# Optimization experiments

Hardware: AMD Instinct MI355X
Metric: run time of the kernel (lower is better)

## Reference

```python
import jax, jax.numpy as jnp
import numpy as np
from jax import lax
from jax.scipy.special import logsumexp

N = 1024   # keypoints image 0
M = 1024   # keypoints image 1
D = 256    # descriptor dim
H = 4      # attention heads
L = 18     # GNN layers ('self','cross')*9
ITERS = 100
KENC = [4, 32, 64, 128, 256]


def conv1(x, w, b):
    # 1x1 Conv1d == channel matmul: x [b,c,n], w [o,c], b [o]
    return jnp.einsum('oc,bcn->bon', w, x) + b[None, :, None]


def inorm(x, eps=1e-5):
    # InstanceNorm1d (affine=False): normalize over length per (b, c)
    m = jnp.mean(x, axis=-1, keepdims=True)
    v = jnp.var(x, axis=-1, keepdims=True)
    return (x - m) * lax.rsqrt(v + eps)


def attention_block(x, src, pw, pb, mw, mb):
    b, d, _ = x.shape
    dh = d // H
    q = conv1(x, pw[0], pb[0]).reshape(b, dh, H, -1)
    k = conv1(src, pw[1], pb[1]).reshape(b, dh, H, -1)
    v = conv1(src, pw[2], pb[2]).reshape(b, dh, H, -1)
    s = jnp.einsum('bdhn,bdhm->bhnm', q, k) / (dh ** 0.5)
    p = jax.nn.softmax(s, axis=-1)
    o = jnp.einsum('bhnm,bdhm->bdhn', p, v).reshape(b, d, -1)
    return conv1(o, mw, mb)


def prop(x, src, i, Pw, Pb, Mw, Mb, W0, B0, W1, B1):
    msg = attention_block(x, src, Pw[i], Pb[i], Mw[i], Mb[i])
    h = jnp.concatenate([x, msg], axis=1)          # [b, 2D, n]
    h = jax.nn.relu(inorm(conv1(h, W0[i], B0[i])))
    return conv1(h, W1[i], B1[i])


def sinkhorn(Z, log_mu, log_nu, iters):
    def step(carry, _):
        u, v = carry
        u = log_mu - logsumexp(Z + v[:, None, :], axis=2)
        v = log_nu - logsumexp(Z + u[:, :, None], axis=1)
        return (u, v), None
    init = (jnp.zeros_like(log_mu), jnp.zeros_like(log_nu))
    (u, v), _ = lax.scan(jax.checkpoint(step), init, None, length=iters)
    return Z + u[:, :, None] + v[:, None, :]


def log_optimal_transport(scores, alpha, iters):
    b, m, n = scores.shape
    bins0 = jnp.broadcast_to(alpha, (b, m, 1))
    bins1 = jnp.broadcast_to(alpha, (b, 1, n))
    binsA = jnp.broadcast_to(alpha, (b, 1, 1))
    couplings = jnp.concatenate([
        jnp.concatenate([scores, bins0], axis=-1),
        jnp.concatenate([bins1, binsA], axis=-1)], axis=1)  # [b, m+1, n+1]
    norm = np.float32(-np.log(m + n))
    log_mu = jnp.concatenate([jnp.full((m,), norm, scores.dtype),
                              jnp.array([np.log(n)], scores.dtype) + norm])
    log_nu = jnp.concatenate([jnp.full((n,), norm, scores.dtype),
                              jnp.array([np.log(m)], scores.dtype) + norm])
    log_mu = jnp.broadcast_to(log_mu[None], (b, m + 1))
    log_nu = jnp.broadcast_to(log_nu[None], (b, n + 1))
    Z = sinkhorn(couplings, log_mu, log_nu, iters)
    return Z - norm


def setup_inputs() -> dict:
    key = jax.random.key(0)
    ks = iter(jax.random.split(key, 64))
    w = lambda shape, s=0.02: jax.random.normal(next(ks), shape, jnp.float32) * s
    inp = {
        'keypoints0': jax.random.normal(next(ks), (1, N, 3), jnp.float32),
        'keypoints1': jax.random.normal(next(ks), (1, M, 3), jnp.float32),
        'descriptors0': jax.random.normal(next(ks), (1, D, N), jnp.float32),
        'descriptors1': jax.random.normal(next(ks), (1, D, M), jnp.float32),
        'scores0': jax.random.uniform(next(ks), (1, N), jnp.float32),
        'scores1': jax.random.uniform(next(ks), (1, M), jnp.float32),
    }
    for i in range(4):
        inp[f'kenc_w{i}'] = w((KENC[i + 1], KENC[i]), 0.1)
        inp[f'kenc_b{i}'] = jnp.zeros((KENC[i + 1],), jnp.float32)
    inp['gnn_proj_w'] = w((L, 3, D, D))
    inp['gnn_proj_b'] = jnp.zeros((L, 3, D), jnp.float32)
    inp['gnn_merge_w'] = w((L, D, D))
    inp['gnn_merge_b'] = jnp.zeros((L, D), jnp.float32)
    inp['gnn_mlp_w0'] = w((L, 2 * D, 2 * D))
    inp['gnn_mlp_b0'] = jnp.zeros((L, 2 * D), jnp.float32)
    inp['gnn_mlp_w1'] = w((L, D, 2 * D))
    inp['gnn_mlp_b1'] = jnp.zeros((L, D), jnp.float32)
    inp['final_w'] = w((D, D))
    inp['final_b'] = jnp.zeros((D,), jnp.float32)
    inp['bin_score'] = jnp.float32(1.0)
    return inp


def reference(keypoints0, keypoints1, descriptors0, descriptors1, scores0, scores1,
              kenc_w0, kenc_b0, kenc_w1, kenc_b1, kenc_w2, kenc_b2, kenc_w3, kenc_b3,
              gnn_proj_w, gnn_proj_b, gnn_merge_w, gnn_merge_b,
              gnn_mlp_w0, gnn_mlp_b0, gnn_mlp_w1, gnn_mlp_b1,
              final_w, final_b, bin_score):
    def kenc(kpts, sc):
        h = jnp.concatenate([jnp.swapaxes(kpts, 1, 2), sc[:, None, :]], axis=1)  # [b,4,n]
        h = jax.nn.relu(inorm(conv1(h, kenc_w0, kenc_b0)))
        h = jax.nn.relu(inorm(conv1(h, kenc_w1, kenc_b1)))
        h = jax.nn.relu(inorm(conv1(h, kenc_w2, kenc_b2)))
        return conv1(h, kenc_w3, kenc_b3)

    d0 = descriptors0 + kenc(keypoints0, scores0)
    d1 = descriptors1 + kenc(keypoints1, scores1)
    for i in range(L):  # even: self, odd: cross
        cross = (i % 2 == 1)
        s0 = d1 if cross else d0
        s1 = d0 if cross else d1
        delta0 = prop(d0, s0, i, gnn_proj_w, gnn_proj_b, gnn_merge_w, gnn_merge_b,
                      gnn_mlp_w0, gnn_mlp_b0, gnn_mlp_w1, gnn_mlp_b1)
        delta1 = prop(d1, s1, i, gnn_proj_w, gnn_proj_b, gnn_merge_w, gnn_merge_b,
                      gnn_mlp_w0, gnn_mlp_b0, gnn_mlp_w1, gnn_mlp_b1)
        d0, d1 = d0 + delta0, d1 + delta1
    md0 = conv1(d0, final_w, final_b)
    md1 = conv1(d1, final_w, final_b)
    scores = jnp.einsum('bdn,bdm->bnm', md0, md1) / (D ** 0.5)
    return log_optimal_transport(scores, bin_score, ITERS)
```

## Files before the change

kernel.cpp:

```cpp
#include <hip/hip_runtime.h>
#include <cstddef>

#define TPB 256

typedef _Float16 f16;
typedef _Float16 f16x4 __attribute__((ext_vector_type(4)));
typedef _Float16 f16x8 __attribute__((ext_vector_type(8)));
typedef float f32x4 __attribute__((ext_vector_type(4)));

__device__ __forceinline__ float block_sum(float v, float* red) {
  int tid = threadIdx.x;
  red[tid] = v; __syncthreads();
#pragma unroll
  for (int off = 128; off > 0; off >>= 1) {
    if (tid < off) red[tid] += red[tid + off];
    __syncthreads();
  }
  float r = red[0];
  __syncthreads();
  return r;
}

__global__ __launch_bounds__(TPB) void build_h0(const float* __restrict__ kp0,
                                                const float* __restrict__ kp1,
                                                const float* __restrict__ sc0,
                                                const float* __restrict__ sc1,
                                                float* __restrict__ h0) {
  int n = blockIdx.x * TPB + threadIdx.x;
  int im = blockIdx.y;
  const float* kp = im ? kp1 : kp0;
  const float* sc = im ? sc1 : sc0;
  float* h = h0 + (size_t)im * 4096;
  h[n]        = kp[n * 3 + 0];
  h[1024 + n] = kp[n * 3 + 1];
  h[2048 + n] = kp[n * 3 + 2];
  h[3072 + n] = sc[n];
}

template<bool NORMRELU, bool RESID>
__global__ __launch_bounds__(TPB) void chanconv(const float* __restrict__ W,
                                                const float* __restrict__ bias,
                                                const float* __restrict__ in, long instride,
                                                const float* res0, const float* res1,
                                                float* __restrict__ out, long outstride, int C) {
  int o = blockIdx.x, im = blockIdx.y, tid = threadIdx.x;
  const float* inp = in + (long)im * instride;
  __shared__ float Ws[128];
  __shared__ float red[TPB];
  for (int c = tid; c < C; c += TPB) Ws[c] = W[(long)o * C + c];
  __syncthreads();
  float b = bias[o];
  float4 acc = {b, b, b, b};
  for (int c = 0; c < C; ++c) {
    float w = Ws[c];
    float4 v = *(const float4*)(inp + (long)c * 1024 + tid * 4);
    acc.x += w * v.x; acc.y += w * v.y; acc.z += w * v.z; acc.w += w * v.w;
  }
  float* orow = out + (long)im * outstride + (long)o * 1024;
  if (NORMRELU) {
    float s = acc.x + acc.y + acc.z + acc.w;
    float mean = block_sum(s, red) * (1.f / 1024.f);
    float dx = acc.x - mean, dy = acc.y - mean, dz = acc.z - mean, dw = acc.w - mean;
    float var = block_sum(dx * dx + dy * dy + dz * dz + dw * dw, red) * (1.f / 1024.f);
    float rstd = rsqrtf(var + 1e-5f);
    float4 o4 = {fmaxf(dx * rstd, 0.f), fmaxf(dy * rstd, 0.f),
                 fmaxf(dz * rstd, 0.f), fmaxf(dw * rstd, 0.f)};
    *(float4*)(orow + tid * 4) = o4;
  } else {
    if (RESID) {
      const float* res = im ? res1 : res0;
      float4 r = *(const float4*)(res + (long)o * 1024 + tid * 4);
      acc.x += r.x; acc.y += r.y; acc.z += r.z; acc.w += r.w;
    }
    *(float4*)(orow + tid * 4) = acc;
  }
}

struct GBH {
  const void* A; const void* B; const void* B2; void* C;
  const float* bias; const float* res; const float* mu; const float* rs;
  void* o2a; void* o2b; int coff; int pad;
};
struct GB16 { GBH g[16]; };

#define F_BNORM   1
#define F_BCONCAT 2
#define F_BADD    4
#define F_CD16    8
#define F_RES     16
#define F_OUT2    32
#define F_CSCAT   64

template<int BN, int ASRC, int BSRC, int FLAGS>
__global__ __launch_bounds__(TPB) void gemmh(GB16 gbs, int K, int lda, int ldb,
                                             int ldc, float alpha, int ksplit) {
  constexpr int WN = BN / 2;
  constexpr int NFR = WN / 16;
  GBH g = gbs.g[blockIdx.z];
  const int tid = threadIdx.x;
  const int lane = tid & 63, wid = tid >> 6;
  const int wm = wid >> 1, wn = wid & 1;
  const int m0 = blockIdx.y * 64, n0 = blockIdx.x * BN;
  __shared__ f16 As[64][36];
  __shared__ f16 Bs[BN][36];
  f32x4 acc[2][NFR];
#pragma unroll
  for (int i = 0; i < 2; ++i)
#pragma unroll
    for (int j = 0; j < NFR; ++j) acc[i][j] = (f32x4){0.f, 0.f, 0.f, 0.f};

  for (int k0 = 0; k0 < K; k0 += 32) {
    if constexpr (ASRC == 0) {
      const int m = tid >> 2, k4 = (tid & 3) * 8;
      const float* ap = (const float*)g.A + (long)(m0 + m) * lda + k0 + k4;
      float4 u0 = *(const float4*)ap, u1 = *(const float4*)(ap + 4);
      f16x4 h0 = {(f16)u0.x, (f16)u0.y, (f16)u0.z, (f16)u0.w};
      f16x4 h1 = {(f16)u1.x, (f16)u1.y, (f16)u1.z, (f16)u1.w};
      *(f16x4*)&As[m][k4] = h0;
      *(f16x4*)&As[m][k4 + 4] = h1;
    } else if constexpr (ASRC == 1) {
      const int k = tid >> 3, mg = (tid & 7) * 8;
      const f16* ap = (const f16*)g.A + (long)(k0 + k) * lda + m0 + mg;
      f16x8 h = *(const f16x8*)ap;
#pragma unroll
      for (int j = 0; j < 8; ++j) As[mg + j][k] = h[j];
    } else {
      const int m = tid >> 2, k4 = (tid & 3) * 8;
      const f16* ap = (const f16*)g.A + (long)(m0 + m) * lda + k0 + k4;
      f16x8 h = *(const f16x8*)ap;
      const float M = g.mu[m0 + m], Iv = g.rs[m0 + m];
      f16x4 h0, h1;
#pragma unroll
      for (int j = 0; j < 4; ++j) h0[j] = (f16)(__expf((float)h[j] - M) * Iv);
#pragma unroll
      for (int j = 0; j < 4; ++j) h1[j] = (f16)(__expf((float)h[j + 4] - M) * Iv);
      *(f16x4*)&As[m][k4] = h0;
      *(f16x4*)&As[m][k4 + 4] = h1;
    }
#pragma unroll
    for (int r = 0; r < BN / 64; ++r) {
      if constexpr (BSRC == 0) {
        const int k = tid >> 3, ng = (tid & 7) * 8 + r * 64;
        const int kg = k0 + k;
        const float* bp;
        if constexpr ((FLAGS & F_BCONCAT) != 0)
          bp = (kg < ksplit) ? ((const float*)g.B + (long)kg * ldb)
                             : ((const float*)g.B2 + (long)(kg - ksplit) * ldb);
        else
          bp = (const float*)g.B + (long)kg * ldb;
        float4 u0 = *(const float4*)(bp + n0 + ng);
        float4 u1 = *(const float4*)(bp + n0 + ng + 4);
        Bs[ng + 0][k] = (f16)u0.x; Bs[ng + 1][k] = (f16)u0.y;
        Bs[ng + 2][k] = (f16)u0.z; Bs[ng + 3][k] = (f16)u0.w;
        Bs[ng + 4][k] = (f16)u1.x; Bs[ng + 5][k] = (f16)u1.y;
        Bs[ng + 6][k] = (f16)u1.z; Bs[ng + 7][k] = (f16)u1.w;
      } else if constexpr (BSRC == 1) {
        const int k = tid >> 3, ng = (tid & 7) * 8 + r * 64;
        const int kg = k0 + k;
        f16x8 h = *(const f16x8*)((const f16*)g.B + (long)kg * ldb + n0 + ng);
        if constexpr ((FLAGS & F_BNORM) != 0) {
          const float mu = g.mu[kg], rs = g.rs[kg];
#pragma unroll
          for (int j = 0; j < 8; ++j)
            h[j] = (f16)fmaxf(((float)h[j] - mu) * rs, 0.f);
        }
#pragma unroll
        for (int j = 0; j < 8; ++j) Bs[ng + j][k] = h[j];
      } else {
        const int n = (tid >> 2) + r * 64, k4 = (tid & 3) * 8;
        const f16* bp = (const f16*)g.B + (long)(n0 + n) * ldb + k0 + k4;
        f16x8 h = *(const f16x8*)bp;
        if constexpr ((FLAGS & F_BADD) != 0) {
          f16x8 h2 = *(const f16x8*)((const f16*)g.B2 + (long)(n0 + n) * ldb + k0 + k4);
          h = h + h2;
        }
        f16x4 h0 = {h[0], h[1], h[2], h[3]};
        f16x4 h1 = {h[4], h[5], h[6], h[7]};
        *(f16x4*)&Bs[n][k4] = h0;
        *(f16x4*)&Bs[n][k4 + 4] = h1;
      }
    }
    __syncthreads();
#pragma unroll
    for (int ks = 0; ks < 2; ++ks) {
      const int kof = ks * 16 + ((lane >> 4) << 2);
      f16x4 a[2], b[NFR];
      a[0] = *(const f16x4*)&As[wm * 32 + (lane & 15)][kof];
      a[1] = *(const f16x4*)&As[wm * 32 + 16 + (lane & 15)][kof];
#pragma unroll
      for (int fn = 0; fn < NFR; ++fn)
        b[fn] = *(const f16x4*)&Bs[wn * WN + fn * 16 + (lane & 15)][kof];
#pragma unroll
      for (int fm = 0; fm < 2; ++fm)
#pragma unroll
        for (int fn = 0; fn < NFR; ++fn)
          acc[fm][fn] = __builtin_amdgcn_mfma_f32_16x16x16f16(a[fm], b[fn], acc[fm][fn], 0, 0, 0);
    }
    __syncthreads();
  }

  const int r0 = (lane >> 4) << 2, cn = lane & 15;
#pragma unroll
  for (int fm = 0; fm < 2; ++fm) {
#pragma unroll
    for (int r = 0; r < 4; ++r) {
      const int m = m0 + wm * 32 + fm * 16 + r0 + r;
      const float bi = g.bias ? g.bias[m] : 0.f;
#pragma unroll
      for (int fn = 0; fn < NFR; ++fn) {
        const int n = n0 + wn * WN + fn * 16 + cn;
        float v = acc[fm][fn][r] * alpha + bi;
        if constexpr ((FLAGS & F_RES) != 0) v += g.res[(long)m * ldc + n];
        if constexpr ((FLAGS & F_OUT2) != 0) {
          ((float*)g.C)[(long)m * 1028 + n] = v;
          ((f16*)g.o2a)[(long)m * 1028 + n] = (f16)v;
          ((f16*)g.o2b)[(long)n * 1028 + m] = (f16)v;
        } else if constexpr ((FLAGS & F_CSCAT) != 0) {
          ((f16*)g.C)[(long)m * ldc + g.coff + 4 * n] = (f16)v;
        } else if constexpr ((FLAGS & F_CD16) != 0) {
          ((f16*)g.C)[(long)m * ldc + n] = (f16)v;
        } else {
          ((float*)g.C)[(long)m * ldc + n] = v;
        }
      }
    }
  }
}

__global__ __launch_bounds__(TPB) void rowlse_h(const f16* __restrict__ S,
                                                float* __restrict__ Mrow,
                                                float* __restrict__ Inv) {
  int row = blockIdx.x * 4 + (threadIdx.x >> 6);
  int lane = threadIdx.x & 63;
  const f16x8* p = (const f16x8*)(S + (long)row * 1024);
  f16x8 v0 = p[lane], v1 = p[lane + 64];
  float m = -1e30f;
#pragma unroll
  for (int j = 0; j < 8; ++j)
    m = fmaxf(m, fmaxf((float)v0[j], (float)v1[j]));
#pragma unroll
  for (int off = 32; off > 0; off >>= 1) m = fmaxf(m, __shfl_xor(m, off));
  float s = 0.f;
#pragma unroll
  for (int j = 0; j < 8; ++j)
    s += __expf((float)v0[j] - m) + __expf((float)v1[j] - m);
#pragma unroll
  for (int off = 32; off > 0; off >>= 1) s += __shfl_xor(s, off);
  if (lane == 0) { Mrow[row] = m; Inv[row] = 1.f / s; }
}

__global__ __launch_bounds__(TPB) void rowstats2_h(const f16* __restrict__ t,
                                                   float* __restrict__ mu,
                                                   float* __restrict__ rs) {
  int row = blockIdx.x * 4 + (threadIdx.x >> 6);
  int lane = threadIdx.x & 63;
  const f16x8* p = (const f16x8*)(t + (long)row * 1024);
  f16x8 v0 = p[lane], v1 = p[lane + 64];
  float s = 0.f, s2 = 0.f;
#pragma unroll
  for (int j = 0; j < 8; ++j) {
    float a = (float)v0[j], b = (float)v1[j];
    s += a + b; s2 += a * a + b * b;
  }
#pragma unroll
  for (int off = 32; off > 0; off >>= 1) { s += __shfl_xor(s, off); s2 += __shfl_xor(s2, off); }
  if (lane == 0) {
    float mean = s * (1.f / 1024.f);
    mu[row] = mean;
    rs[row] = rsqrtf(fmaxf(s2 * (1.f / 1024.f) - mean * mean, 0.f) + 1e-5f);
  }
}

#define NORMC  (-7.62461899f)
#define LOGN   (6.93147181f)
#define LOG_MN (7.62461899f)
#define ZLD    1028
#define SINKB  64

__global__ __launch_bounds__(TPB) void fill_bins(float* __restrict__ Z,
                                                 const float* __restrict__ alpha_p,
                                                 float* __restrict__ vb,
                                                 unsigned* __restrict__ bar) {
  float a = *alpha_p;
  int t = blockIdx.x * TPB + threadIdx.x;
  if (t < ZLD) vb[t] = 0.f;
  if (t == 0) *bar = 0u;
  if (t <= 1024) {
    Z[(long)t * ZLD + 1024] = a;
    Z[(long)1024 * ZLD + t] = a;
  }
}

__device__ __forceinline__ float llc_load(const float* p) {
  return __hip_atomic_load(p, __ATOMIC_RELAXED, __HIP_MEMORY_SCOPE_AGENT);
}
__device__ __forceinline__ void llc_store(float* p, float v) {
  __hip_atomic_store(p, v, __ATOMIC_RELAXED, __HIP_MEMORY_SCOPE_AGENT);
}

__device__ __forceinline__ void gridbar(unsigned* __restrict__ bar, unsigned gen) {
  __syncthreads();
  if (threadIdx.x == 0) {
    __hip_atomic_fetch_add(bar, 1u, __ATOMIC_RELAXED, __HIP_MEMORY_SCOPE_AGENT);
    const unsigned target = gen * SINKB;
    while (__hip_atomic_load(bar, __ATOMIC_RELAXED, __HIP_MEMORY_SCOPE_AGENT) < target) {}
  }
  asm volatile("" ::: "memory");
  __syncthreads();
}

__device__ __forceinline__ void sink_half(const f16x8 zreg[4][2],
                                          const float* __restrict__ w,
                                          float* __restrict__ out,
                                          int gw, int lane, float alpha) {
  float vv[16];
#pragma unroll
  for (int t = 0; t < 16; ++t) vv[t] = llc_load(w + lane + 64 * t);
  const float w1024 = llc_load(w + 1024);
  const float binv = alpha + w1024;

#pragma unroll
  for (int r = 0; r < 4; ++r) {
    float val[16];
    float m = binv;
#pragma unroll
    for (int t = 0; t < 16; ++t) {
      val[t] = (float)zreg[r][t >> 3][t & 7] + vv[t];
      m = fmaxf(m, val[t]);
    }
#pragma unroll
    for (int off = 32; off > 0; off >>= 1) m = fmaxf(m, __shfl_xor(m, off));
    float s = 0.f;
#pragma unroll
    for (int t = 0; t < 16; ++t) s += __expf(val[t] - m);
#pragma unroll
    for (int off = 32; off > 0; off >>= 1) s += __shfl_xor(s, off);
    s += __expf(binv - m);
    if (lane == 0) out[gw + 256 * r] = 0.f;
    if (lane == 0) llc_store(out + gw + 256 * r, NORMC - (m + logf(s)));
  }

  if (gw == 0) {
    float m = w1024;
#pragma unroll
    for (int t = 0; t < 16; ++t) m = fmaxf(m, vv[t]);
#pragma unroll
    for (int off = 32; off > 0; off >>= 1) m = fmaxf(m, __shfl_xor(m, off));
    float s = 0.f;
#pragma unroll
    for (int t = 0; t < 16; ++t) s += __expf(vv[t] - m);
#pragma unroll
    for (int off = 32; off > 0; off >>= 1) s += __shfl_xor(s, off);
    s += __expf(w1024 - m);
    if (lane == 0)
      llc_store(out + 1024, NORMC + LOGN - (alpha + m + logf(s)));
  }
}

__global__ __launch_bounds__(TPB) void sink_persist(const f16* __restrict__ Zh,
                                                    const f16* __restrict__ Zth,
                                                    float* __restrict__ ub,
                                                    float* __restrict__ vb,
                                                    unsigned* __restrict__ bar,
                                                    const float* __restrict__ alpha_p) {
  const int lane = threadIdx.x & 63;
  const int gw = blockIdx.x * 4 + (threadIdx.x >> 6);
  const float alpha = *alpha_p;

  f16x8 zr[4][2], zt[4][2];
#pragma unroll
  for (int r = 0; r < 4; ++r) {
    const long row = gw + 256 * r;
    const f16* zp = Zh + row * ZLD;
    const f16* ztp = Zth + row * ZLD;
#pragma unroll
    for (int h = 0; h < 2; ++h)
#pragma unroll
      for (int j = 0; j < 8; ++j) {
        zr[r][h][j] = zp[lane + 64 * (8 * h + j)];
        zt[r][h][j] = ztp[lane + 64 * (8 * h + j)];
      }
  }

  unsigned gen = 0;
#pragma unroll 1
  for (int it = 0; it < 100; ++it) {
    sink_half(zr, vb, ub, gw, lane, alpha);
    gridbar(bar, ++gen);
    sink_half(zt, ub, vb, gw, lane, alpha);
    gridbar(bar, ++gen);
  }
}

__global__ __launch_bounds__(TPB) void assemble(const float* __restrict__ Z,
                                                const float* __restrict__ u,
                                                const float* __restrict__ v,
                                                float* __restrict__ out) {
  int idx = blockIdx.x * TPB + threadIdx.x;
  if (idx < 1025 * 1025) {
    int i = idx / 1025;
    int j = idx - i * 1025;
    out[idx] = Z[(long)i * ZLD + j] + u[i] + v[j] + LOG_MN;
  }
}

static inline GBH mkgb(const void* A, const void* B, void* C,
                       const float* bias = nullptr, const void* B2 = nullptr,
                       const float* res = nullptr,
                       const float* mu = nullptr, const float* rs = nullptr,
                       int coff = 0, void* o2a = nullptr, void* o2b = nullptr) {
  GBH g; g.A = A; g.B = B; g.B2 = B2; g.C = C; g.bias = bias; g.res = res;
  g.mu = mu; g.rs = rs; g.o2a = o2a; g.o2b = o2b; g.coff = coff; g.pad = 0;
  return g;
}

extern "C" void kernel_launch(void* const* d_in, const int* in_sizes, int n_in,
                              void* d_out, int out_size, void* d_ws, size_t ws_size,
                              hipStream_t stream) {
  const float* kp0     = (const float*)d_in[0];
  const float* kp1     = (const float*)d_in[1];
  const float* desc0   = (const float*)d_in[2];
  const float* desc1   = (const float*)d_in[3];
  const float* sc0     = (const float*)d_in[4];
  const float* sc1     = (const float*)d_in[5];
  const float* kw[4]   = {(const float*)d_in[6], (const float*)d_in[8],
                          (const float*)d_in[10], (const float*)d_in[12]};
  const float* kb[4]   = {(const float*)d_in[7], (const float*)d_in[9],
                          (const float*)d_in[11], (const float*)d_in[13]};
  const float* proj_w  = (const float*)d_in[14];
  const float* proj_b  = (const float*)d_in[15];
  const float* merge_w = (const float*)d_in[16];
  const float* merge_b = (const float*)d_in[17];
  const float* mlp_w0  = (const float*)d_in[18];
  const float* mlp_b0  = (const float*)d_in[19];
  const float* mlp_w1  = (const float*)d_in[20];
  const float* mlp_b1  = (const float*)d_in[21];
  const float* final_w = (const float*)d_in[22];
  const float* final_b = (const float*)d_in[23];
  const float* alpha_p = (const float*)d_in[24];

  float* p = (float*)d_ws;
  float* dA  = p; p += 524288;
  float* dB  = p; p += 524288;
  float* h0  = p; p += 8192;
  float* hb1 = p; p += 262144;
  float* hb2 = p; p += 131072;
  float* msg = p; p += 524288;
  float* muA = p; p += 1024;
  float* rsA = p; p += 1024;
  float* Mrw = p; p += 8192;
  float* Inv = p; p += 8192;
  float* Zb  = p; p += 1053700;
  float* ub  = p; p += 1028;
  float* vb  = p; p += 1028;
  unsigned* bar = (unsigned*)p; p += 4;
  f16* qkvh = (f16*)p; p += 786432;
  f16* Sh   = (f16*)p; p += 4194304;
  f16* oAh  = (f16*)p; p += 262144;
  f16* oBh  = (f16*)p; p += 262144;
  f16* tbh  = (f16*)p; p += 524288;
  f16* mdbh = (f16*)p; p += 262144;
  f16* Zh   = (f16*)p; p += 526852;
  f16* Zth  = (f16*)p; p += 526852;
  size_t need_bytes = (size_t)(p - (float*)d_ws) * sizeof(float);
  if (ws_size < need_bytes) return;

  const long DSTR = 262144;

  build_h0<<<dim3(4, 2), TPB, 0, stream>>>(kp0, kp1, sc0, sc1, h0);
  chanconv<true, false><<<dim3(32, 2),  TPB, 0, stream>>>(kw[0], kb[0], h0,  4096,   nullptr, nullptr, hb1, 32768,  4);
  chanconv<true, false><<<dim3(64, 2),  TPB, 0, stream>>>(kw[1], kb[1], hb1, 32768,  nullptr, nullptr, hb2, 65536,  32);
  chanconv<true, false><<<dim3(128, 2), TPB, 0, stream>>>(kw[2], kb[2], hb2, 65536,  nullptr, nullptr, hb1, 131072, 64);
  chanconv<false, true><<<dim3(256, 2), TPB, 0, stream>>>(kw[3], kb[3], hb1, 131072, desc0,   desc1,   dA,  DSTR,   128);

  float* dc = dA;
  float* dn = dB;
  for (int i = 0; i < 18; ++i) {
    bool cross = (i & 1) != 0;
    const float* xs[2] = {dc, dc + DSTR};
    const float* ss2[2] = {cross ? xs[1] : xs[0], cross ? xs[0] : xs[1]};

    {
      GB16 gb{};
      for (int im = 0; im < 2; ++im)
        for (int pp = 0; pp < 3; ++pp)
          gb.g[im * 3 + pp] = mkgb(proj_w + (size_t)(i * 3 + pp) * 65536,
                                   (pp == 0 ? xs[im] : ss2[im]),
                                   qkvh + (size_t)(im * 3 + pp) * DSTR,
                                   proj_b + (size_t)(i * 3 + pp) * 256);
      gemmh<128, 0, 0, F_CD16><<<dim3(8, 4, 6), TPB, 0, stream>>>(
          gb, 256, 256, 1024, 1024, 1.f, 0);
    }
    {
      GB16 gb{};
      for (int im = 0; im < 2; ++im)
        for (int h = 0; h < 4; ++h)
          gb.g[im * 4 + h] = mkgb(qkvh + (size_t)(im * 3 + 0) * DSTR + h * 1024,
                                  qkvh + (size_t)(im * 3 + 1) * DSTR + h * 1024,
                                  Sh + (size_t)(im * 4 + h) * 1048576);
      gemmh<128, 1, 1, F_CD16><<<dim3(8, 16, 8), TPB, 0, stream>>>(
          gb, 64, 4096, 4096, 1024, 0.125f, 0);
    }
    rowlse_h<<<2048, TPB, 0, stream>>>(Sh, Mrw, Inv);
    {
      GB16 gb{};
      for (int kh = 0; kh < 2; ++kh)
        for (int imh = 0; imh < 8; ++imh) {
          int im = imh >> 2, h = imh & 3;
          gb.g[kh * 8 + imh] = mkgb(Sh + (size_t)imh * 1048576 + kh * 512,
                                    qkvh + (size_t)(im * 3 + 2) * DSTR + h * 1024 + kh * 512,
                                    (kh ? oBh : oAh) + (size_t)im * 262144,
                                    nullptr, nullptr, nullptr,
                                    Mrw + imh * 1024, Inv + imh * 1024, h);
        }
      gemmh<64, 2, 2, F_CD16 | F_CSCAT><<<dim3(1, 16, 16), TPB, 0, stream>>>(
          gb, 512, 1024, 4096, 256, 1.f, 0);
    }
    {
      GB16 gb{};
      for (int im = 0; im < 2; ++im)
        gb.g[im] = mkgb(merge_w + (size_t)i * 65536, oAh + (size_t)im * 262144,
                        msg + (size_t)im * DSTR, merge_b + (size_t)i * 256,
                        oBh + (size_t)im * 262144);
      gemmh<64, 0, 2, F_BADD><<<dim3(16, 4, 2), TPB, 0, stream>>>(
          gb, 256, 256, 256, 1024, 1.f, 0);
    }
    {
      GB16 gb{};
      for (int im = 0; im < 2; ++im)
        gb.g[im] = mkgb(mlp_w0 + (size_t)i * 262144, xs[im],
                        tbh + (size_t)im * 524288, mlp_b0 + (size_t)i * 512,
                        msg + (size_t)im * DSTR);
      gemmh<64, 0, 0, F_BCONCAT | F_CD16><<<dim3(16, 8, 2), TPB, 0, stream>>>(
          gb, 512, 512, 1024, 1024, 1.f, 256);
    }
    rowstats2_h<<<256, TPB, 0, stream>>>(tbh, muA, rsA);
    {
      GB16 gb{};
      for (int im = 0; im < 2; ++im)
        gb.g[im] = mkgb(mlp_w1 + (size_t)i * 131072, tbh + (size_t)im * 524288,
                        dn + (size_t)im * DSTR, mlp_b1 + (size_t)i * 256,
                        nullptr, xs[im],
                        muA + (size_t)im * 512, rsA + (size_t)im * 512);
      gemmh<64, 0, 1, F_BNORM | F_RES><<<dim3(16, 4, 2), TPB, 0, stream>>>(
          gb, 512, 512, 1024, 1024, 1.f, 0);
    }
    float* tmp = dc; dc = dn; dn = tmp;
  }

  {
    GB16 gb{};
    for (int im = 0; im < 2; ++im)
      gb.g[im] = mkgb(final_w, dc + (size_t)im * DSTR, mdbh + (size_t)im * 262144,
                      final_b);
    gemmh<64, 0, 0, F_CD16><<<dim3(16, 4, 2), TPB, 0, stream>>>(
        gb, 256, 256, 1024, 1024, 1.f, 0);
  }
  {
    GB16 gb{};
    gb.g[0] = mkgb(mdbh, mdbh + 262144, Zb, nullptr, nullptr, nullptr,
                   nullptr, nullptr, 0, Zh, Zth);
    gemmh<64, 1, 1, F_OUT2><<<dim3(16, 16, 1), TPB, 0, stream>>>(
        gb, 256, 1024, 1024, ZLD, 0.0625f, 0);
  }
  fill_bins<<<5, TPB, 0, stream>>>(Zb, alpha_p, vb, bar);

  sink_persist<<<SINKB, TPB, 0, stream>>>(Zh, Zth, ub, vb, bar, alpha_p);

  assemble<<<4105, TPB, 0, stream>>>(Zb, ub, vb, (float*)d_out);
}
```

Baseline: 2.485 ms.

## Replace Sinkhorn grid barrier with generation-tagged dataflow slots

```diff
diff --git a/kernel.cpp b/kernel.cpp
--- a/kernel.cpp
+++ b/kernel.cpp
@@ -7,6 +7,7 @@
 typedef _Float16 f16x4 __attribute__((ext_vector_type(4)));
 typedef _Float16 f16x8 __attribute__((ext_vector_type(8)));
 typedef float f32x4 __attribute__((ext_vector_type(4)));
+typedef unsigned long long u64;
 
 __device__ __forceinline__ float block_sum(float v, float* red) {
   int tid = threadIdx.x;
@@ -277,47 +278,61 @@
 #define ZLD    1028
 #define SINKB  64
 
+__device__ __forceinline__ u64 slot_load(const u64* p) {
+  return __hip_atomic_load(p, __ATOMIC_RELAXED, __HIP_MEMORY_SCOPE_AGENT);
+}
+__device__ __forceinline__ void slot_store(u64* p, float v, unsigned gen) {
+  union { float f; unsigned u; } c; c.f = v;
+  u64 x = ((u64)gen << 32) | (u64)c.u;
+  __hip_atomic_store(p, x, __ATOMIC_RELAXED, __HIP_MEMORY_SCOPE_AGENT);
+}
+__device__ __forceinline__ float slot_val(u64 x) {
+  union { unsigned u; float f; } c; c.u = (unsigned)x;
+  return c.f;
+}
+
 __global__ __launch_bounds__(TPB) void fill_bins(float* __restrict__ Z,
                                                  const float* __restrict__ alpha_p,
-                                                 float* __restrict__ vb,
-                                                 unsigned* __restrict__ bar) {
+                                                 u64* __restrict__ uS,
+                                                 u64* __restrict__ vS) {
   float a = *alpha_p;
   int t = blockIdx.x * TPB + threadIdx.x;
-  if (t < ZLD) vb[t] = 0.f;
-  if (t == 0) *bar = 0u;
   if (t <= 1024) {
     Z[(long)t * ZLD + 1024] = a;
     Z[(long)1024 * ZLD + t] = a;
-  }
-}
-
-__device__ __forceinline__ float llc_load(const float* p) {
-  return __hip_atomic_load(p, __ATOMIC_RELAXED, __HIP_MEMORY_SCOPE_AGENT);
-}
-__device__ __forceinline__ void llc_store(float* p, float v) {
-  __hip_atomic_store(p, v, __ATOMIC_RELAXED, __HIP_MEMORY_SCOPE_AGENT);
-}
-
-__device__ __forceinline__ void gridbar(unsigned* __restrict__ bar, unsigned gen) {
-  __syncthreads();
-  if (threadIdx.x == 0) {
-    __hip_atomic_fetch_add(bar, 1u, __ATOMIC_RELAXED, __HIP_MEMORY_SCOPE_AGENT);
-    const unsigned target = gen * SINKB;
-    while (__hip_atomic_load(bar, __ATOMIC_RELAXED, __HIP_MEMORY_SCOPE_AGENT) < target) {}
-  }
-  asm volatile("" ::: "memory");
-  __syncthreads();
+    slot_store(uS + t, 0.f, 0u);
+    slot_store(vS + t, 0.f, 0u);
+  }
+}
+
+__device__ __forceinline__ void poll_vec(const u64* __restrict__ w, unsigned gen,
+                                         int lane, float vv[16], float& w1024) {
+  u64 raw[16]; u64 rb;
+  bool ok = false;
+  while (!ok) {
+    ok = true;
+#pragma unroll
+    for (int t = 0; t < 16; ++t) raw[t] = slot_load(w + lane + 64 * t);
+    rb = slot_load(w + 1024);
+#pragma unroll
+    for (int t = 0; t < 16; ++t)
+      if ((unsigned)(raw[t] >> 32) != gen) ok = false;
+    if ((unsigned)(rb >> 32) != gen) ok = false;
+  }
+#pragma unroll
+  for (int t = 0; t < 16; ++t) vv[t] = slot_val(raw[t]);
+  w1024 = slot_val(rb);
 }
 
 __device__ __forceinline__ void sink_half(const f16x8 zreg[4][2],
-                                          const float* __restrict__ w,
-                                          float* __restrict__ out,
-                                          int gw, int lane, float alpha) {
-  float vv[16];
-#pragma unroll
-  for (int t = 0; t < 16; ++t) vv[t] = llc_load(w + lane + 64 * t);
-  const float w1024 = llc_load(w + 1024);
+                                          const u64* __restrict__ w,
+                                          u64* __restrict__ out,
+                                          unsigned rgen, int gw, int lane,
+                                          float alpha) {
+  float vv[16]; float w1024;
+  poll_vec(w, rgen, lane, vv, w1024);
   const float binv = alpha + w1024;
+  const unsigned wgen = rgen + 1;
 
 #pragma unroll
   for (int r = 0; r < 4; ++r) {
@@ -336,8 +351,8 @@
 #pragma unroll
     for (int off = 32; off > 0; off >>= 1) s += __shfl_xor(s, off);
     s += __expf(binv - m);
-    if (lane == 0) out[gw + 256 * r] = 0.f;
-    if (lane == 0) llc_store(out + gw + 256 * r, NORMC - (m + logf(s)));
+    if (lane == 0)
+      slot_store(out + gw + 256 * r, NORMC - (m + logf(s)), wgen);
   }
 
   if (gw == 0) {
@@ -353,15 +368,14 @@
     for (int off = 32; off > 0; off >>= 1) s += __shfl_xor(s, off);
     s += __expf(w1024 - m);
     if (lane == 0)
-      llc_store(out + 1024, NORMC + LOGN - (alpha + m + logf(s)));
+      slot_store(out + 1024, NORMC + LOGN - (alpha + m + logf(s)), wgen);
   }
 }
 
 __global__ __launch_bounds__(TPB) void sink_persist(const f16* __restrict__ Zh,
                                                     const f16* __restrict__ Zth,
-                                                    float* __restrict__ ub,
-                                                    float* __restrict__ vb,
-                                                    unsigned* __restrict__ bar,
+                                                    u64* __restrict__ uS,
+                                                    u64* __restrict__ vS,
                                                     const float* __restrict__ alpha_p) {
   const int lane = threadIdx.x & 63;
   const int gw = blockIdx.x * 4 + (threadIdx.x >> 6);
@@ -385,22 +399,20 @@
   unsigned gen = 0;
 #pragma unroll 1
   for (int it = 0; it < 100; ++it) {
-    sink_half(zr, vb, ub, gw, lane, alpha);
-    gridbar(bar, ++gen);
-    sink_half(zt, ub, vb, gw, lane, alpha);
-    gridbar(bar, ++gen);
+    sink_half(zr, vS, uS, gen, gw, lane, alpha);  ++gen;
+    sink_half(zt, uS, vS, gen, gw, lane, alpha);  ++gen;
   }
 }
 
 __global__ __launch_bounds__(TPB) void assemble(const float* __restrict__ Z,
-                                                const float* __restrict__ u,
-                                                const float* __restrict__ v,
+                                                const u64* __restrict__ uS,
+                                                const u64* __restrict__ vS,
                                                 float* __restrict__ out) {
   int idx = blockIdx.x * TPB + threadIdx.x;
   if (idx < 1025 * 1025) {
     int i = idx / 1025;
     int j = idx - i * 1025;
-    out[idx] = Z[(long)i * ZLD + j] + u[i] + v[j] + LOG_MN;
+    out[idx] = Z[(long)i * ZLD + j] + slot_val(uS[i]) + slot_val(vS[j]) + LOG_MN;
   }
 }
 
@@ -451,9 +463,8 @@
   float* Mrw = p; p += 8192;
   float* Inv = p; p += 8192;
   float* Zb  = p; p += 1053700;
-  float* ub  = p; p += 1028;
-  float* vb  = p; p += 1028;
-  unsigned* bar = (unsigned*)p; p += 4;
+  u64* uS = (u64*)p; p += 2050;
+  u64* vS = (u64*)p; p += 2050;
   f16* qkvh = (f16*)p; p += 786432;
   f16* Sh   = (f16*)p; p += 4194304;
   f16* oAh  = (f16*)p; p += 262144;
@@ -563,9 +574,9 @@
     gemmh<64, 1, 1, F_OUT2><<<dim3(16, 16, 1), TPB, 0, stream>>>(
         gb, 256, 1024, 1024, ZLD, 0.0625f, 0);
   }
-  fill_bins<<<5, TPB, 0, stream>>>(Zb, alpha_p, vb, bar);
-
-  sink_persist<<<SINKB, TPB, 0, stream>>>(Zh, Zth, ub, vb, bar, alpha_p);
-
-  assemble<<<4105, TPB, 0, stream>>>(Zb, ub, vb, (float*)d_out);
-}
+  fill_bins<<<5, TPB, 0, stream>>>(Zb, alpha_p, uS, vS);
+
+  sink_persist<<<SINKB, TPB, 0, stream>>>(Zh, Zth, uS, vS, alpha_p);
+
+  assemble<<<4105, TPB, 0, stream>>>(Zb, uS, vS, (float*)d_out);
+}
```

Measured after the change: 2.661 ms. 1.07x slower.

## Stage Sinkhorn potentials through LDS with 64-bit loads; add BM=32 GEMM tiles

Applied to the files above, without the earlier changes.

```diff
diff --git a/kernel.cpp b/kernel.cpp
--- a/kernel.cpp
+++ b/kernel.cpp
@@ -7,6 +7,7 @@
 typedef _Float16 f16x4 __attribute__((ext_vector_type(4)));
 typedef _Float16 f16x8 __attribute__((ext_vector_type(8)));
 typedef float f32x4 __attribute__((ext_vector_type(4)));
+typedef unsigned long long u64;
 
 __device__ __forceinline__ float block_sum(float v, float* red) {
   int tid = threadIdx.x;
@@ -91,17 +92,19 @@
 #define F_OUT2    32
 #define F_CSCAT   64
 
-template<int BN, int ASRC, int BSRC, int FLAGS>
+template<int BM, int BN, int ASRC, int BSRC, int FLAGS>
 __global__ __launch_bounds__(TPB) void gemmh(GB16 gbs, int K, int lda, int ldb,
                                              int ldc, float alpha, int ksplit) {
-  constexpr int WN = BN / 2;
+  constexpr int WM = BM / 32;
+  constexpr int NWN = 4 / WM;
+  constexpr int WN = BN / NWN;
   constexpr int NFR = WN / 16;
   GBH g = gbs.g[blockIdx.z];
   const int tid = threadIdx.x;
   const int lane = tid & 63, wid = tid >> 6;
-  const int wm = wid >> 1, wn = wid & 1;
-  const int m0 = blockIdx.y * 64, n0 = blockIdx.x * BN;
-  __shared__ f16 As[64][36];
+  const int wm = wid / NWN, wn = wid % NWN;
+  const int m0 = blockIdx.y * BM, n0 = blockIdx.x * BN;
+  __shared__ f16 As[BM][36];
   __shared__ f16 Bs[BN][36];
   f32x4 acc[2][NFR];
 #pragma unroll
@@ -111,13 +114,21 @@
 
   for (int k0 = 0; k0 < K; k0 += 32) {
     if constexpr (ASRC == 0) {
-      const int m = tid >> 2, k4 = (tid & 3) * 8;
-      const float* ap = (const float*)g.A + (long)(m0 + m) * lda + k0 + k4;
-      float4 u0 = *(const float4*)ap, u1 = *(const float4*)(ap + 4);
-      f16x4 h0 = {(f16)u0.x, (f16)u0.y, (f16)u0.z, (f16)u0.w};
-      f16x4 h1 = {(f16)u1.x, (f16)u1.y, (f16)u1.z, (f16)u1.w};
-      *(f16x4*)&As[m][k4] = h0;
-      *(f16x4*)&As[m][k4 + 4] = h1;
+      if constexpr (BM == 64) {
+        const int m = tid >> 2, k4 = (tid & 3) * 8;
+        const float* ap = (const float*)g.A + (long)(m0 + m) * lda + k0 + k4;
+        float4 u0 = *(const float4*)ap, u1 = *(const float4*)(ap + 4);
+        f16x4 h0 = {(f16)u0.x, (f16)u0.y, (f16)u0.z, (f16)u0.w};
+        f16x4 h1 = {(f16)u1.x, (f16)u1.y, (f16)u1.z, (f16)u1.w};
+        *(f16x4*)&As[m][k4] = h0;
+        *(f16x4*)&As[m][k4 + 4] = h1;
+      } else {
+        const int m = tid >> 3, k4 = (tid & 7) * 4;
+        const float* ap = (const float*)g.A + (long)(m0 + m) * lda + k0 + k4;
+        float4 u0 = *(const float4*)ap;
+        f16x4 h0 = {(f16)u0.x, (f16)u0.y, (f16)u0.z, (f16)u0.w};
+        *(f16x4*)&As[m][k4] = h0;
+      }
     } else if constexpr (ASRC == 1) {
       const int k = tid >> 3, mg = (tid & 7) * 8;
       const f16* ap = (const f16*)g.A + (long)(k0 + k) * lda + m0 + mg;
@@ -277,25 +288,31 @@
 #define ZLD    1028
 #define SINKB  64
 
+__device__ __forceinline__ u64 llc_load64(const u64* p) {
+  return __hip_atomic_load(p, __ATOMIC_RELAXED, __HIP_MEMORY_SCOPE_AGENT);
+}
+__device__ __forceinline__ void llc_store64(u64* p, u64 v) {
+  __hip_atomic_store(p, v, __ATOMIC_RELAXED, __HIP_MEMORY_SCOPE_AGENT);
+}
+__device__ __forceinline__ void llc_store32(float* p, float v) {
+  __hip_atomic_store(p, v, __ATOMIC_RELAXED, __HIP_MEMORY_SCOPE_AGENT);
+}
+__device__ __forceinline__ u64 pack2(float a, float b) {
+  union { float f[2]; u64 x; } c; c.f[0] = a; c.f[1] = b; return c.x;
+}
+
 __global__ __launch_bounds__(TPB) void fill_bins(float* __restrict__ Z,
                                                  const float* __restrict__ alpha_p,
-                                                 float* __restrict__ vb,
+                                                 float* __restrict__ vF,
                                                  unsigned* __restrict__ bar) {
   float a = *alpha_p;
   int t = blockIdx.x * TPB + threadIdx.x;
-  if (t < ZLD) vb[t] = 0.f;
+  if (t < ZLD) vF[t] = 0.f;
   if (t == 0) *bar = 0u;
   if (t <= 1024) {
     Z[(long)t * ZLD + 1024] = a;
     Z[(long)1024 * ZLD + t] = a;
   }
-}
-
-__device__ __forceinline__ float llc_load(const float* p) {
-  return __hip_atomic_load(p, __ATOMIC_RELAXED, __HIP_MEMORY_SCOPE_AGENT);
-}
-__device__ __forceinline__ void llc_store(float* p, float v) {
-  __hip_atomic_store(p, v, __ATOMIC_RELAXED, __HIP_MEMORY_SCOPE_AGENT);
 }
 
 __device__ __forceinline__ void gridbar(unsigned* __restrict__ bar, unsigned gen) {
@@ -312,13 +329,22 @@
 __device__ __forceinline__ void sink_half(const f16x8 zreg[4][2],
                                           const float* __restrict__ w,
                                           float* __restrict__ out,
-                                          int gw, int lane, float alpha) {
+                                          int tid, int gw, int lane,
+                                          float alpha, float* __restrict__ lds) {
+  for (int s = tid; s < 513; s += TPB) {
+    u64 x = llc_load64((const u64*)w + s);
+    union { u64 x; float f[2]; } c; c.x = x;
+    lds[2 * s] = c.f[0];
+    lds[2 * s + 1] = c.f[1];
+  }
+  __syncthreads();
   float vv[16];
 #pragma unroll
-  for (int t = 0; t < 16; ++t) vv[t] = llc_load(w + lane + 64 * t);
-  const float w1024 = llc_load(w + 1024);
+  for (int t = 0; t < 16; ++t) vv[t] = lds[lane + 64 * t];
+  const float w1024 = lds[1024];
   const float binv = alpha + w1024;
 
+  float res[4];
 #pragma unroll
   for (int r = 0; r < 4; ++r) {
     float val[16];
@@ -336,9 +362,10 @@
 #pragma unroll
     for (int off = 32; off > 0; off >>= 1) s += __shfl_xor(s, off);
     s += __expf(binv - m);
-    if (lane == 0) out[gw + 256 * r] = 0.f;
-    if (lane == 0) llc_store(out + gw + 256 * r, NORMC - (m + logf(s)));
-  }
+    res[r] = NORMC - (m + logf(s));
+  }
+  if (lane < 2)
+    llc_store64((u64*)(out + 4 * gw) + lane, pack2(res[2 * lane], res[2 * lane + 1]));
 
   if (gw == 0) {
     float m = w1024;
@@ -353,24 +380,26 @@
     for (int off = 32; off > 0; off >>= 1) s += __shfl_xor(s, off);
     s += __expf(w1024 - m);
     if (lane == 0)
-      llc_store(out + 1024, NORMC + LOGN - (alpha + m + logf(s)));
+      llc_store32(out + 1024, NORMC + LOGN - (alpha + m + logf(s)));
   }
 }
 
 __global__ __launch_bounds__(TPB) void sink_persist(const f16* __restrict__ Zh,
                                                     const f16* __restrict__ Zth,
-                                                    float* __restrict__ ub,
-                                                    float* __restrict__ vb,
+                                                    float* __restrict__ uF,
+                                                    float* __restrict__ vF,
                                                     unsigned* __restrict__ bar,
                                                     const float* __restrict__ alpha_p) {
-  const int lane = threadIdx.x & 63;
-  const int gw = blockIdx.x * 4 + (threadIdx.x >> 6);
+  __shared__ float lds[ZLD];
+  const int tid = threadIdx.x;
+  const int lane = tid & 63;
+  const int gw = blockIdx.x * 4 + (tid >> 6);
   const float alpha = *alpha_p;
 
   f16x8 zr[4][2], zt[4][2];
 #pragma unroll
   for (int r = 0; r < 4; ++r) {
-    const long row = gw + 256 * r;
+    const long row = 4 * gw + r;
     const f16* zp = Zh + row * ZLD;
     const f16* ztp = Zth + row * ZLD;
 #pragma unroll
@@ -385,9 +414,9 @@
   unsigned gen = 0;
 #pragma unroll 1
   for (int it = 0; it < 100; ++it) {
-    sink_half(zr, vb, ub, gw, lane, alpha);
+    sink_half(zr, vF, uF, tid, gw, lane, alpha, lds);
     gridbar(bar, ++gen);
-    sink_half(zt, ub, vb, gw, lane, alpha);
+    sink_half(zt, uF, vF, tid, gw, lane, alpha, lds);
     gridbar(bar, ++gen);
   }
 }
@@ -451,8 +480,8 @@
   float* Mrw = p; p += 8192;
   float* Inv = p; p += 8192;
   float* Zb  = p; p += 1053700;
-  float* ub  = p; p += 1028;
-  float* vb  = p; p += 1028;
+  float* uF  = p; p += 1028;
+  float* vF  = p; p += 1028;
   unsigned* bar = (unsigned*)p; p += 4;
   f16* qkvh = (f16*)p; p += 786432;
   f16* Sh   = (f16*)p; p += 4194304;
@@ -488,7 +517,7 @@
                                    (pp == 0 ? xs[im] : ss2[im]),
                                    qkvh + (size_t)(im * 3 + pp) * DSTR,
                                    proj_b + (size_t)(i * 3 + pp) * 256);
-      gemmh<128, 0, 0, F_CD16><<<dim3(8, 4, 6), TPB, 0, stream>>>(
+      gemmh<32, 128, 0, 0, F_CD16><<<dim3(8, 8, 6), TPB, 0, stream>>>(
           gb, 256, 256, 1024, 1024, 1.f, 0);
     }
     {
@@ -498,7 +527,7 @@
           gb.g[im * 4 + h] = mkgb(qkvh + (size_t)(im * 3 + 0) * DSTR + h * 1024,
                                   qkvh + (size_t)(im * 3 + 1) * DSTR + h * 1024,
                                   Sh + (size_t)(im * 4 + h) * 1048576);
-      gemmh<128, 1, 1, F_CD16><<<dim3(8, 16, 8), TPB, 0, stream>>>(
+      gemmh<64, 128, 1, 1, F_CD16><<<dim3(8, 16, 8), TPB, 0, stream>>>(
           gb, 64, 4096, 4096, 1024, 0.125f, 0);
     }
     rowlse_h<<<2048, TPB, 0, stream>>>(Sh, Mrw, Inv);
@@ -513,7 +542,7 @@
                                     nullptr, nullptr, nullptr,
                                     Mrw + imh * 1024, Inv + imh * 1024, h);
         }
-      gemmh<64, 2, 2, F_CD16 | F_CSCAT><<<dim3(1, 16, 16), TPB, 0, stream>>>(
+      gemmh<64, 64, 2, 2, F_CD16 | F_CSCAT><<<dim3(1, 16, 16), TPB, 0, stream>>>(
           gb, 512, 1024, 4096, 256, 1.f, 0);
     }
     {
@@ -522,7 +551,7 @@
         gb.g[im] = mkgb(merge_w + (size_t)i * 65536, oAh + (size_t)im * 262144,
                         msg + (size_t)im * DSTR, merge_b + (size_t)i * 256,
                         oBh + (size_t)im * 262144);
-      gemmh<64, 0, 2, F_BADD><<<dim3(16, 4, 2), TPB, 0, stream>>>(
+      gemmh<32, 64, 0, 2, F_BADD><<<dim3(16, 8, 2), TPB, 0, stream>>>(
           gb, 256, 256, 256, 1024, 1.f, 0);
     }
     {
@@ -531,7 +560,7 @@
         gb.g[im] = mkgb(mlp_w0 + (size_t)i * 262144, xs[im],
                         tbh + (size_t)im * 524288, mlp_b0 + (size_t)i * 512,
                         msg + (size_t)im * DSTR);
-      gemmh<64, 0, 0, F_BCONCAT | F_CD16><<<dim3(16, 8, 2), TPB, 0, stream>>>(
+      gemmh<64, 64, 0, 0, F_BCONCAT | F_CD16><<<dim3(16, 8, 2), TPB, 0, stream>>>(
           gb, 512, 512, 1024, 1024, 1.f, 256);
     }
     rowstats2_h<<<256, TPB, 0, stream>>>(tbh, muA, rsA);
@@ -542,7 +571,7 @@
                         dn + (size_t)im * DSTR, mlp_b1 + (size_t)i * 256,
                         nullptr, xs[im],
                         muA + (size_t)im * 512, rsA + (size_t)im * 512);
-      gemmh<64, 0, 1, F_BNORM | F_RES><<<dim3(16, 4, 2), TPB, 0, stream>>>(
+      gemmh<32, 64, 0, 1, F_BNORM | F_RES><<<dim3(16, 8, 2), TPB, 0, stream>>>(
           gb, 512, 512, 1024, 1024, 1.f, 0);
     }
     float* tmp = dc; dc = dn; dn = tmp;
@@ -553,19 +582,19 @@
     for (int im = 0; im < 2; ++im)
       gb.g[im] = mkgb(final_w, dc + (size_t)im * DSTR, mdbh + (size_t)im * 262144,
                       final_b);
-    gemmh<64, 0, 0, F_CD16><<<dim3(16, 4, 2), TPB, 0, stream>>>(
+    gemmh<32, 64, 0, 0, F_CD16><<<dim3(16, 8, 2), TPB, 0, stream>>>(
         gb, 256, 256, 1024, 1024, 1.f, 0);
   }
   {
     GB16 gb{};
     gb.g[0] = mkgb(mdbh, mdbh + 262144, Zb, nullptr, nullptr, nullptr,
                    nullptr, nullptr, 0, Zh, Zth);
-    gemmh<64, 1, 1, F_OUT2><<<dim3(16, 16, 1), TPB, 0, stream>>>(
+    gemmh<64, 64, 1, 1, F_OUT2><<<dim3(16, 16, 1), TPB, 0, stream>>>(
         gb, 256, 1024, 1024, ZLD, 0.0625f, 0);
   }
-  fill_bins<<<5, TPB, 0, stream>>>(Zb, alpha_p, vb, bar);
-
-  sink_persist<<<SINKB, TPB, 0, stream>>>(Zh, Zth, ub, vb, bar, alpha_p);
-
-  assemble<<<4105, TPB, 0, stream>>>(Zb, ub, vb, (float*)d_out);
-}
+  fill_bins<<<5, TPB, 0, stream>>>(Zb, alpha_p, vF, bar);
+
+  sink_persist<<<SINKB, TPB, 0, stream>>>(Zh, Zth, uF, vF, bar, alpha_p);
+
+  assemble<<<4105, TPB, 0, stream>>>(Zb, uF, vF, (float*)d_out);
+}
```

Result: faster. 2.283 ms (-8.1%).
